# Kernel tuning notes

Measured on AMD Instinct MI355X. Metric: run time of the kernel, lower is better.

The kernel has to match this reference:

```python
import jax, jax.numpy as jnp
import numpy as np

N_USERS = 200000
N_ITEMS = 50000
N_INTER = 2_000_000
LATENT_DIM = 64
N_LAYERS = 3
BATCH = 4096


def setup_inputs() -> dict:
    rng = np.random.default_rng(0)
    u = rng.integers(0, N_USERS, N_INTER)
    i = rng.integers(0, N_ITEMS, N_INTER)
    # symmetric bipartite adjacency: user->item and item->user blocks
    rows = np.concatenate([u, i + N_USERS])
    cols = np.concatenate([i + N_USERS, u])
    n = N_USERS + N_ITEMS
    deg = np.bincount(rows, minlength=n).astype(np.float32)
    d_inv_sqrt = np.power(deg + 1e-9, -0.5)
    d_inv_sqrt[np.isinf(d_inv_sqrt)] = 0.0
    vals = (d_inv_sqrt[rows] * d_inv_sqrt[cols]).astype(np.float32)  # D^-1/2 A D^-1/2

    key = jax.random.key(0)
    # xavier-uniform-ish init for the embedding table
    bound = float(np.sqrt(6.0 / (n + LATENT_DIM)))
    embed_weight = jax.random.uniform(key, (n, LATENT_DIM), jnp.float32, -bound, bound)

    users = jnp.asarray(rng.integers(0, N_USERS, BATCH), dtype=jnp.int64)
    pos_items = jnp.asarray(rng.integers(0, N_ITEMS, BATCH), dtype=jnp.int64)
    neg_items = jnp.asarray(rng.integers(0, N_ITEMS, BATCH), dtype=jnp.int64)

    return {
        "embed_weight": embed_weight,
        "adj_rows": jnp.asarray(rows, dtype=jnp.int32),
        "adj_cols": jnp.asarray(cols, dtype=jnp.int32),
        "adj_vals": jnp.asarray(vals),
        "users": users,
        "pos_items": pos_items,
        "neg_items": neg_items,
    }


def reference(embed_weight, adj_rows, adj_cols, adj_vals, users, pos_items, neg_items):
    n = embed_weight.shape[0]

    def spmm(x):
        # out[r] += vals * x[c]  (normalized adjacency times embeddings)
        return jax.ops.segment_sum(adj_vals[:, None] * x[adj_cols], adj_rows, num_segments=n)

    acc = embed_weight  # running sum over layers (layer 0 = initial embeddings)
    e = embed_weight
    for _ in range(N_LAYERS):
        e = spmm(e)
        acc = acc + e
    mean_emb = acc / (N_LAYERS + 1)

    final_user, final_item = mean_emb[:N_USERS], mean_emb[N_USERS:]
    init_user, init_item = embed_weight[:N_USERS], embed_weight[N_USERS:]

    return (
        final_user[users],
        final_item[pos_items],
        final_item[neg_items],
        init_user[users],
        init_item[pos_items],
        init_item[neg_items],
    )
```

## Files before the change

### kernel.cpp

```cpp
#include <hip/hip_runtime.h>

#define N_USERS 200000
#define N_ITEMS 50000
#define NTOT    (N_USERS + N_ITEMS)
#define DIM     64
#define BATCH   4096

#define RB      256
#define NB      ((NTOT + RB - 1) / RB)
#define TILE    8192
#define CAP     15360

__global__ void coarse_hist(const int* __restrict__ rows, int* __restrict__ bCnt, int nE) {
    __shared__ int h[NB];
    for (int b = threadIdx.x; b < NB; b += blockDim.x) h[b] = 0;
    __syncthreads();
    const int t  = blockIdx.x * blockDim.x + threadIdx.x;
    const int nT = gridDim.x * blockDim.x;
    const int n4 = nE >> 2;
    for (int i = t; i < n4; i += nT) {
        const int4 r4 = reinterpret_cast<const int4*>(rows)[i];
        atomicAdd(&h[r4.x >> 8], 1);
        atomicAdd(&h[r4.y >> 8], 1);
        atomicAdd(&h[r4.z >> 8], 1);
        atomicAdd(&h[r4.w >> 8], 1);
    }
    for (int e = (n4 << 2) + t; e < nE; e += nT) atomicAdd(&h[rows[e] >> 8], 1);
    __syncthreads();
    for (int b = threadIdx.x; b < NB; b += blockDim.x) {
        const int c = h[b];
        if (c) atomicAdd(&bCnt[b], c);
    }
}

__global__ void bucket_scan(const int* __restrict__ bCnt, int* __restrict__ bStart,
                            int* __restrict__ bCur) {
    __shared__ int sc[1024];
    const int t = threadIdx.x;
    const int v = (t < NB) ? bCnt[t] : 0;
    sc[t] = v;
    __syncthreads();
    int incl = v;
    for (int s = 1; s < 1024; s <<= 1) {
        const int add = (t >= s) ? sc[t - s] : 0;
        __syncthreads();
        incl += add;
        sc[t] = incl;
        __syncthreads();
    }
    if (t < NB) {
        const int excl = incl - v;
        bStart[t] = excl;
        bCur[t]   = excl;
        if (t == NB - 1) bStart[NB] = incl;
    }
}

__global__ __launch_bounds__(256) void phase_a(const int* __restrict__ rows,
                                               const int* __restrict__ cols,
                                               int* __restrict__ bCur,
                                               int* __restrict__ entA, int nE) {
    __shared__ int cnt[NB];
    __shared__ int base[NB];
    const int tid = threadIdx.x;
    for (int b = tid; b < NB; b += 256) cnt[b] = 0;
    __syncthreads();
    const int tb = blockIdx.x * TILE;
    const int te = min(tb + TILE, nE);
    for (int e = tb + tid; e < te; e += 256) atomicAdd(&cnt[rows[e] >> 8], 1);
    __syncthreads();
    for (int b = tid; b < NB; b += 256) {
        const int c = cnt[b];
        if (c) base[b] = atomicAdd(&bCur[b], c);
        cnt[b] = 0;
    }
    __syncthreads();
    for (int e = tb + tid; e < te; e += 256) {
        const int r = rows[e];
        const int b = r >> 8;
        const int rank = atomicAdd(&cnt[b], 1);
        entA[base[b] + rank] = cols[e] | ((r & (RB - 1)) << 18);
    }
}

__global__ __launch_bounds__(256) void phase_b(const int* __restrict__ entA,
                                               const int* __restrict__ bStart,
                                               int* __restrict__ ccol,
                                               int* __restrict__ P,
                                               float* __restrict__ dis) {
    __shared__ int cnt2[RB];
    __shared__ int sc[RB];
    __shared__ int cur[RB];
    __shared__ int srt[CAP];
    const int b   = blockIdx.x;
    const int tid = threadIdx.x;
    const int beg = bStart[b], end = bStart[b + 1];
    const int n   = end - beg;
    cnt2[tid] = 0;
    __syncthreads();
    for (int i = tid; i < n; i += 256) atomicAdd(&cnt2[entA[beg + i] >> 18], 1);
    __syncthreads();
    const int v = cnt2[tid];
    sc[tid] = v;
    __syncthreads();
    int incl = v;
    for (int s = 1; s < 256; s <<= 1) {
        const int add = (tid >= s) ? sc[tid - s] : 0;
        __syncthreads();
        incl += add;
        sc[tid] = incl;
        __syncthreads();
    }
    cur[tid] = incl - v;
    const int row = b * RB + tid;
    if (row < NTOT) {
        P[row]   = beg + incl;
        dis[row] = 1.0f / sqrtf((float)v + 1e-9f);
    }
    __syncthreads();
    if (n <= CAP) {
        for (int i = tid; i < n; i += 256) {
            const int e = entA[beg + i];
            const int pos = atomicAdd(&cur[e >> 18], 1);
            srt[pos] = e & 0x3FFFF;
        }
        __syncthreads();
        for (int i = tid; i < n; i += 256) ccol[beg + i] = srt[i];
    } else {
        for (int i = tid; i < n; i += 256) {
            const int e = entA[beg + i];
            const int pos = atomicAdd(&cur[e >> 18], 1);
            ccol[beg + pos] = e & 0x3FFFF;
        }
    }
}

__global__ __launch_bounds__(256) void spmm_csr(const float* __restrict__ x,
                                                const int* __restrict__ P,
                                                const int* __restrict__ ccol,
                                                const float* __restrict__ dis,
                                                float* __restrict__ y) {
    const int lane = threadIdx.x & 63;
    const int wid  = blockIdx.x * 4 + (threadIdx.x >> 6);
    if (wid >= NTOT) return;
    const int beg = (wid == 0) ? 0 : P[wid - 1];
    const int end = P[wid];
    float acc = 0.f;
    int e = beg;
    for (; e + 8 <= end; e += 8) {
        int c[8]; float w[8], xv[8];
        #pragma unroll
        for (int k = 0; k < 8; ++k) c[k] = ccol[e + k];
        #pragma unroll
        for (int k = 0; k < 8; ++k) w[k] = dis[c[k]];
        #pragma unroll
        for (int k = 0; k < 8; ++k) xv[k] = x[(size_t)c[k] * DIM + lane];
        #pragma unroll
        for (int k = 0; k < 8; ++k) acc += w[k] * xv[k];
    }
    for (; e < end; ++e) {
        const int c = ccol[e];
        acc += dis[c] * x[(size_t)c * DIM + lane];
    }
    acc *= dis[wid];
    y[(size_t)wid * DIM + lane] = acc;
}

__global__ __launch_bounds__(256) void spmm_rows_out(const float* __restrict__ x,
                                                     const int* __restrict__ P,
                                                     const int* __restrict__ ccol,
                                                     const float* __restrict__ dis,
                                                     const int* __restrict__ users,
                                                     const int* __restrict__ pos,
                                                     const int* __restrict__ neg,
                                                     float* __restrict__ out) {
    const int lane = threadIdx.x & 63;
    const int wid  = blockIdx.x * 4 + (threadIdx.x >> 6);
    if (wid >= 3 * BATCH) return;
    const int s = wid / BATCH;
    const int j = wid - s * BATCH;
    const int row = (s == 0) ? users[j] : (s == 1) ? pos[j] + N_USERS : neg[j] + N_USERS;
    const int beg = (row == 0) ? 0 : P[row - 1];
    const int end = P[row];
    float acc = 0.f;
    int e = beg;
    for (; e + 4 <= end; e += 4) {
        int c[4]; float w[4], xv[4];
        #pragma unroll
        for (int k = 0; k < 4; ++k) c[k] = ccol[e + k];
        #pragma unroll
        for (int k = 0; k < 4; ++k) w[k] = dis[c[k]];
        #pragma unroll
        for (int k = 0; k < 4; ++k) xv[k] = x[(size_t)c[k] * DIM + lane];
        #pragma unroll
        for (int k = 0; k < 4; ++k) acc += w[k] * xv[k];
    }
    for (; e < end; ++e) {
        const int c = ccol[e];
        acc += dis[c] * x[(size_t)c * DIM + lane];
    }
    acc *= dis[row];
    const size_t o = (size_t)(s * BATCH + j) * DIM + lane;
    out[o] = (out[o] + acc) * 0.25f;
}

__global__ void spmm_scatter(const float* __restrict__ x, const int* __restrict__ rows,
                             const int* __restrict__ cols, const float* __restrict__ vals,
                             float* __restrict__ y, int nE) {
    const int lane = threadIdx.x & 63;
    const int wid  = blockIdx.x * (blockDim.x >> 6) + (threadIdx.x >> 6);
    const int nw   = gridDim.x * (blockDim.x >> 6);
    for (int e = wid; e < nE; e += nw)
        atomicAdd(&y[(size_t)rows[e] * DIM + lane], vals[e] * x[(size_t)cols[e] * DIM + lane]);
}

__global__ void init_out(const float* __restrict__ emb, const int* __restrict__ users,
                         const int* __restrict__ pos, const int* __restrict__ neg,
                         float* __restrict__ out) {
    const int t = blockIdx.x * blockDim.x + threadIdx.x;
    const int lane = t & 63;
    const int w = t >> 6;
    if (w >= 3 * BATCH) return;
    const int s = w / BATCH;
    const int j = w - s * BATCH;
    const int row = (s == 0) ? users[j] : (s == 1) ? pos[j] + N_USERS : neg[j] + N_USERS;
    const float v = emb[(size_t)row * DIM + lane];
    out[(size_t)(s * BATCH + j) * DIM + lane] = v;
    out[(size_t)((s + 3) * BATCH + j) * DIM + lane] = v;
}

__global__ void gather_addscale(const float* __restrict__ e, const int* __restrict__ users,
                                const int* __restrict__ pos, const int* __restrict__ neg,
                                float* __restrict__ out, float scale) {
    const int t = blockIdx.x * blockDim.x + threadIdx.x;
    const int lane = t & 63;
    const int w = t >> 6;
    if (w >= 3 * BATCH) return;
    const int s = w / BATCH;
    const int j = w - s * BATCH;
    const int row = (s == 0) ? users[j] : (s == 1) ? pos[j] + N_USERS : neg[j] + N_USERS;
    const size_t o = (size_t)(s * BATCH + j) * DIM + lane;
    out[o] = (out[o] + e[(size_t)row * DIM + lane]) * scale;
}

extern "C" void kernel_launch(void* const* d_in, const int* in_sizes, int n_in,
                              void* d_out, int out_size, void* d_ws, size_t ws_size,
                              hipStream_t stream) {
    const float* emb  = (const float*)d_in[0];
    const int*   rows = (const int*)d_in[1];
    const int*   cols = (const int*)d_in[2];
    const float* vals = (const float*)d_in[3];
    const int*   users = (const int*)d_in[4];
    const int*   pos   = (const int*)d_in[5];
    const int*   neg   = (const int*)d_in[6];
    float* out = (float*)d_out;

    const int nE = in_sizes[1];
    auto rup = [](size_t x) { return (x + 255) & ~(size_t)255; };
    const size_t szBuf = rup((size_t)NTOT * DIM * sizeof(float));
    const size_t szCol = rup((size_t)nE * sizeof(int));
    const size_t szP   = rup((size_t)NTOT * sizeof(int));
    const size_t szDis = rup((size_t)NTOT * sizeof(float));
    const size_t szBk  = rup((size_t)(NB + 1) * sizeof(int));

    char* w = (char*)d_ws;
    float* bufA = (float*)w; w += szBuf;
    float* bufB = (float*)w; w += szBuf;
    int* entA   = (int*)bufB;
    int*   ccol = (int*)w;   w += szCol;
    int*   P    = (int*)w;   w += szP;
    float* dis  = (float*)w; w += szDis;
    int* bCnt   = (int*)w;   w += szBk;
    int* bStart = (int*)w;   w += szBk;
    int* bCur   = (int*)w;   w += szBk;
    const size_t need = (size_t)((char*)w - (char*)d_ws);

    const int gatherBlocks = (3 * BATCH * DIM + 255) / 256;

    init_out<<<gatherBlocks, 256, 0, stream>>>(emb, users, pos, neg, out);

    if (ws_size >= need && nE > 0) {
        hipMemsetAsync(bCnt, 0, (size_t)NB * sizeof(int), stream);
        coarse_hist<<<512, 256, 0, stream>>>(rows, bCnt, nE);
        bucket_scan<<<1, 1024, 0, stream>>>(bCnt, bStart, bCur);
        const int nTiles = (nE + TILE - 1) / TILE;
        phase_a<<<nTiles, 256, 0, stream>>>(rows, cols, bCur, entA, nE);
        phase_b<<<NB, 256, 0, stream>>>(entA, bStart, ccol, P, dis);

        const int spmmBlocks = (NTOT + 3) / 4;
        spmm_csr<<<spmmBlocks, 256, 0, stream>>>(emb,  P, ccol, dis, bufA);
        gather_addscale<<<gatherBlocks, 256, 0, stream>>>(bufA, users, pos, neg, out, 1.0f);
        spmm_csr<<<spmmBlocks, 256, 0, stream>>>(bufA, P, ccol, dis, bufB);
        gather_addscale<<<gatherBlocks, 256, 0, stream>>>(bufB, users, pos, neg, out, 1.0f);
        const int rowsBlocks = (3 * BATCH + 3) / 4;
        spmm_rows_out<<<rowsBlocks, 256, 0, stream>>>(bufB, P, ccol, dis, users, pos, neg, out);
    } else {
        const size_t bufBytes = (size_t)NTOT * DIM * sizeof(float);
        hipMemsetAsync(bufA, 0, bufBytes, stream);
        spmm_scatter<<<2048, 256, 0, stream>>>(emb, rows, cols, vals, bufA, nE);
        gather_addscale<<<gatherBlocks, 256, 0, stream>>>(bufA, users, pos, neg, out, 1.0f);
        hipMemsetAsync(bufB, 0, bufBytes, stream);
        spmm_scatter<<<2048, 256, 0, stream>>>(bufA, rows, cols, vals, bufB, nE);
        gather_addscale<<<gatherBlocks, 256, 0, stream>>>(bufB, users, pos, neg, out, 1.0f);
        hipMemsetAsync(bufA, 0, bufBytes, stream);
        spmm_scatter<<<2048, 256, 0, stream>>>(bufB, rows, cols, vals, bufA, nE);
        gather_addscale<<<gatherBlocks, 256, 0, stream>>>(bufA, users, pos, neg, out, 0.25f);
    }
}
```

Baseline: 642.4 us.

## Vectorize SpMM gathers with float4 across four edge groups and sort CSR columns

The CSR SpMM kernels now split each wavefront into four 16-lane groups. Each group loads a whole 64-float row with float4 loads and handles every fourth edge, and a cross-group shuffle reduction combines the partial sums. This raises memory-level parallelism and the width of each gather. Phase_a now reads rows and cols as int4 to cut load instructions in the COO-to-bucket pass. Phase_b adds a per-row serial insertion sort of column indices in shared memory so that gathers hit ascending addresses, which costs extra serial work for high-degree rows and runs only on the in-shared-memory path.

```diff
diff --git a/kernel.cpp b/kernel.cpp
--- a/kernel.cpp
+++ b/kernel.cpp
@@ -67,7 +67,17 @@
     __syncthreads();
     const int tb = blockIdx.x * TILE;
     const int te = min(tb + TILE, nE);
-    for (int e = tb + tid; e < te; e += 256) atomicAdd(&cnt[rows[e] >> 8], 1);
+    const int nv = (te - tb) >> 2;
+    const int4* rows4 = reinterpret_cast<const int4*>(rows + tb);
+    const int4* cols4 = reinterpret_cast<const int4*>(cols + tb);
+    for (int i = tid; i < nv; i += 256) {
+        const int4 r4 = rows4[i];
+        atomicAdd(&cnt[r4.x >> 8], 1);
+        atomicAdd(&cnt[r4.y >> 8], 1);
+        atomicAdd(&cnt[r4.z >> 8], 1);
+        atomicAdd(&cnt[r4.w >> 8], 1);
+    }
+    for (int e = tb + (nv << 2) + tid; e < te; e += 256) atomicAdd(&cnt[rows[e] >> 8], 1);
     __syncthreads();
     for (int b = tid; b < NB; b += 256) {
         const int c = cnt[b];
@@ -75,7 +85,20 @@
         cnt[b] = 0;
     }
     __syncthreads();
-    for (int e = tb + tid; e < te; e += 256) {
+    for (int i = tid; i < nv; i += 256) {
+        const int4 r4 = rows4[i];
+        const int4 c4 = cols4[i];
+        int r, b, rank;
+        r = r4.x; b = r >> 8; rank = atomicAdd(&cnt[b], 1);
+        entA[base[b] + rank] = c4.x | ((r & (RB - 1)) << 18);
+        r = r4.y; b = r >> 8; rank = atomicAdd(&cnt[b], 1);
+        entA[base[b] + rank] = c4.y | ((r & (RB - 1)) << 18);
+        r = r4.z; b = r >> 8; rank = atomicAdd(&cnt[b], 1);
+        entA[base[b] + rank] = c4.z | ((r & (RB - 1)) << 18);
+        r = r4.w; b = r >> 8; rank = atomicAdd(&cnt[b], 1);
+        entA[base[b] + rank] = c4.w | ((r & (RB - 1)) << 18);
+    }
+    for (int e = tb + (nv << 2) + tid; e < te; e += 256) {
         const int r = rows[e];
         const int b = r >> 8;
         const int rank = atomicAdd(&cnt[b], 1);
@@ -111,7 +134,8 @@
         sc[tid] = incl;
         __syncthreads();
     }
-    cur[tid] = incl - v;
+    const int myBeg = incl - v;
+    cur[tid] = myBeg;
     const int row = b * RB + tid;
     if (row < NTOT) {
         P[row]   = beg + incl;
@@ -123,6 +147,16 @@
             const int e = entA[beg + i];
             const int pos = atomicAdd(&cur[e >> 18], 1);
             srt[pos] = e & 0x3FFFF;
+        }
+        __syncthreads();
+        for (int i = 1; i < v; ++i) {
+            const int key = srt[myBeg + i];
+            int j = i - 1;
+            while (j >= 0 && srt[myBeg + j] > key) {
+                srt[myBeg + j + 1] = srt[myBeg + j];
+                --j;
+            }
+            srt[myBeg + j + 1] = key;
         }
         __syncthreads();
         for (int i = tid; i < n; i += 256) ccol[beg + i] = srt[i];
@@ -141,29 +175,42 @@
                                                 const float* __restrict__ dis,
                                                 float* __restrict__ y) {
     const int lane = threadIdx.x & 63;
+    const int sub  = lane & 15;
+    const int grp  = lane >> 4;
     const int wid  = blockIdx.x * 4 + (threadIdx.x >> 6);
     if (wid >= NTOT) return;
     const int beg = (wid == 0) ? 0 : P[wid - 1];
     const int end = P[wid];
-    float acc = 0.f;
-    int e = beg;
-    for (; e + 8 <= end; e += 8) {
-        int c[8]; float w[8], xv[8];
-        #pragma unroll
-        for (int k = 0; k < 8; ++k) c[k] = ccol[e + k];
-        #pragma unroll
-        for (int k = 0; k < 8; ++k) w[k] = dis[c[k]];
-        #pragma unroll
-        for (int k = 0; k < 8; ++k) xv[k] = x[(size_t)c[k] * DIM + lane];
-        #pragma unroll
-        for (int k = 0; k < 8; ++k) acc += w[k] * xv[k];
-    }
-    for (; e < end; ++e) {
+    const float4* x4 = reinterpret_cast<const float4*>(x);
+    float4 acc = make_float4(0.f, 0.f, 0.f, 0.f);
+    int e = beg + grp;
+    for (; e + 12 < end; e += 16) {
+        const int c0 = ccol[e], c1 = ccol[e + 4], c2 = ccol[e + 8], c3 = ccol[e + 12];
+        const float w0 = dis[c0], w1 = dis[c1], w2 = dis[c2], w3 = dis[c3];
+        const float4 v0 = x4[(size_t)c0 * 16 + sub];
+        const float4 v1 = x4[(size_t)c1 * 16 + sub];
+        const float4 v2 = x4[(size_t)c2 * 16 + sub];
+        const float4 v3 = x4[(size_t)c3 * 16 + sub];
+        acc.x += w0 * v0.x + w1 * v1.x + w2 * v2.x + w3 * v3.x;
+        acc.y += w0 * v0.y + w1 * v1.y + w2 * v2.y + w3 * v3.y;
+        acc.z += w0 * v0.z + w1 * v1.z + w2 * v2.z + w3 * v3.z;
+        acc.w += w0 * v0.w + w1 * v1.w + w2 * v2.w + w3 * v3.w;
+    }
+    for (; e < end; e += 4) {
         const int c = ccol[e];
-        acc += dis[c] * x[(size_t)c * DIM + lane];
-    }
-    acc *= dis[wid];
-    y[(size_t)wid * DIM + lane] = acc;
+        const float w = dis[c];
+        const float4 v = x4[(size_t)c * 16 + sub];
+        acc.x += w * v.x; acc.y += w * v.y; acc.z += w * v.z; acc.w += w * v.w;
+    }
+    acc.x += __shfl_xor(acc.x, 16); acc.y += __shfl_xor(acc.y, 16);
+    acc.z += __shfl_xor(acc.z, 16); acc.w += __shfl_xor(acc.w, 16);
+    acc.x += __shfl_xor(acc.x, 32); acc.y += __shfl_xor(acc.y, 32);
+    acc.z += __shfl_xor(acc.z, 32); acc.w += __shfl_xor(acc.w, 32);
+    if (grp == 0) {
+        const float dr = dis[wid];
+        acc.x *= dr; acc.y *= dr; acc.z *= dr; acc.w *= dr;
+        reinterpret_cast<float4*>(y)[(size_t)wid * 16 + sub] = acc;
+    }
 }
 
 __global__ __launch_bounds__(256) void spmm_rows_out(const float* __restrict__ x,
@@ -175,6 +222,8 @@
                                                      const int* __restrict__ neg,
                                                      float* __restrict__ out) {
     const int lane = threadIdx.x & 63;
+    const int sub  = lane & 15;
+    const int grp  = lane >> 4;
     const int wid  = blockIdx.x * 4 + (threadIdx.x >> 6);
     if (wid >= 3 * BATCH) return;
     const int s = wid / BATCH;
@@ -182,26 +231,42 @@
     const int row = (s == 0) ? users[j] : (s == 1) ? pos[j] + N_USERS : neg[j] + N_USERS;
     const int beg = (row == 0) ? 0 : P[row - 1];
     const int end = P[row];
-    float acc = 0.f;
-    int e = beg;
-    for (; e + 4 <= end; e += 4) {
-        int c[4]; float w[4], xv[4];
-        #pragma unroll
-        for (int k = 0; k < 4; ++k) c[k] = ccol[e + k];
-        #pragma unroll
-        for (int k = 0; k < 4; ++k) w[k] = dis[c[k]];
-        #pragma unroll
-        for (int k = 0; k < 4; ++k) xv[k] = x[(size_t)c[k] * DIM + lane];
-        #pragma unroll
-        for (int k = 0; k < 4; ++k) acc += w[k] * xv[k];
-    }
-    for (; e < end; ++e) {
+    const float4* x4 = reinterpret_cast<const float4*>(x);
+    float4 acc = make_float4(0.f, 0.f, 0.f, 0.f);
+    int e = beg + grp;
+    for (; e + 12 < end; e += 16) {
+        const int c0 = ccol[e], c1 = ccol[e + 4], c2 = ccol[e + 8], c3 = ccol[e + 12];
+        const float w0 = dis[c0], w1 = dis[c1], w2 = dis[c2], w3 = dis[c3];
+        const float4 v0 = x4[(size_t)c0 * 16 + sub];
+        const float4 v1 = x4[(size_t)c1 * 16 + sub];
+        const float4 v2 = x4[(size_t)c2 * 16 + sub];
+        const float4 v3 = x4[(size_t)c3 * 16 + sub];
+        acc.x += w0 * v0.x + w1 * v1.x + w2 * v2.x + w3 * v3.x;
+        acc.y += w0 * v0.y + w1 * v1.y + w2 * v2.y + w3 * v3.y;
+        acc.z += w0 * v0.z + w1 * v1.z + w2 * v2.z + w3 * v3.z;
+        acc.w += w0 * v0.w + w1 * v1.w + w2 * v2.w + w3 * v3.w;
+    }
+    for (; e < end; e += 4) {
         const int c = ccol[e];
-        acc += dis[c] * x[(size_t)c * DIM + lane];
-    }
-    acc *= dis[row];
-    const size_t o = (size_t)(s * BATCH + j) * DIM + lane;
-    out[o] = (out[o] + acc) * 0.25f;
+        const float w = dis[c];
+        const float4 v = x4[(size_t)c * 16 + sub];
+        acc.x += w * v.x; acc.y += w * v.y; acc.z += w * v.z; acc.w += w * v.w;
+    }
+    acc.x += __shfl_xor(acc.x, 16); acc.y += __shfl_xor(acc.y, 16);
+    acc.z += __shfl_xor(acc.z, 16); acc.w += __shfl_xor(acc.w, 16);
+    acc.x += __shfl_xor(acc.x, 32); acc.y += __shfl_xor(acc.y, 32);
+    acc.z += __shfl_xor(acc.z, 32); acc.w += __shfl_xor(acc.w, 32);
+    if (grp == 0) {
+        const float dr = dis[row];
+        float4* out4 = reinterpret_cast<float4*>(out);
+        const size_t o = (size_t)(s * BATCH + j) * 16 + sub;
+        float4 ov = out4[o];
+        ov.x = (ov.x + acc.x * dr) * 0.25f;
+        ov.y = (ov.y + acc.y * dr) * 0.25f;
+        ov.z = (ov.z + acc.z * dr) * 0.25f;
+        ov.w = (ov.w + acc.w * dr) * 0.25f;
+        out4[o] = ov;
+    }
 }
 
 __global__ void spmm_scatter(const float* __restrict__ x, const int* __restrict__ rows,
```

Result: slower. 753.7 us (+17.3%).
